# Kernel optimization log

Hardware: AMD Instinct MI355X
Metric: run time of the kernel (lower is better)

Reference implementation:

```python
import jax, jax.numpy as jnp
import numpy as np

N_NODES = 1_000_000
HID = 64
BATCH = 262_144


def _gru_cell(x, h, w_ih, w_hh, b_ih, b_hh):
    # PyTorch GRUCell semantics. w_ih/w_hh: [3H, H]; gate order r, z, n.
    gi = x @ w_ih.T + b_ih
    gh = h @ w_hh.T + b_hh
    i_r, i_z, i_n = jnp.split(gi, 3, axis=-1)
    h_r, h_z, h_n = jnp.split(gh, 3, axis=-1)
    r = jax.nn.sigmoid(i_r + h_r)
    z = jax.nn.sigmoid(i_z + h_z)
    n = jnp.tanh(i_n + r * h_n)
    return (1.0 - z) * n + z * h


def setup_inputs() -> dict:
    key = jax.random.key(0)
    ks = jax.random.split(key, 16)
    H = HID
    s = lambda fan_in: 1.0 / np.sqrt(fan_in)
    return {
        "node_pairs": jax.random.randint(ks[0], (BATCH, 2), 0, N_NODES, dtype=jnp.int64)
        if jax.config.jax_enable_x64 else jax.random.randint(ks[0], (BATCH, 2), 0, N_NODES, dtype=jnp.int32),
        "memory": jax.random.normal(ks[1], (N_NODES, H), dtype=jnp.float32),
        "msg_w1": jax.random.uniform(ks[2], (H, 2 * H), jnp.float32, -s(2 * H), s(2 * H)),
        "msg_b1": jax.random.uniform(ks[3], (H,), jnp.float32, -s(2 * H), s(2 * H)),
        "msg_w2": jax.random.uniform(ks[4], (H, H), jnp.float32, -s(H), s(H)),
        "msg_b2": jax.random.uniform(ks[5], (H,), jnp.float32, -s(H), s(H)),
        "gru_w_ih": jax.random.uniform(ks[6], (3 * H, H), jnp.float32, -s(H), s(H)),
        "gru_w_hh": jax.random.uniform(ks[7], (3 * H, H), jnp.float32, -s(H), s(H)),
        "gru_b_ih": jax.random.uniform(ks[8], (3 * H,), jnp.float32, -s(H), s(H)),
        "gru_b_hh": jax.random.uniform(ks[9], (3 * H,), jnp.float32, -s(H), s(H)),
        "lp_w1": jax.random.uniform(ks[10], (H, 2 * H), jnp.float32, -s(2 * H), s(2 * H)),
        "lp_b1": jax.random.uniform(ks[11], (H,), jnp.float32, -s(2 * H), s(2 * H)),
        "lp_w2": jax.random.uniform(ks[12], (1, H), jnp.float32, -s(H), s(H)),
        "lp_b2": jax.random.uniform(ks[13], (1,), jnp.float32, -s(H), s(H)),
    }


def reference(node_pairs, memory, msg_w1, msg_b1, msg_w2, msg_b2,
              gru_w_ih, gru_w_hh, gru_b_ih, gru_b_hh,
              lp_w1, lp_b1, lp_w2, lp_b2):
    n1_mem = memory[node_pairs[:, 0]]  # [B, H]
    n2_mem = memory[node_pairs[:, 1]]  # [B, H]
    x = jnp.concatenate([n1_mem, n2_mem], axis=1)  # [B, 2H]
    messages = jax.nn.relu(x @ msg_w1.T + msg_b1) @ msg_w2.T + msg_b2  # [B, H]
    n1_upd = _gru_cell(messages, n1_mem, gru_w_ih, gru_w_hh, gru_b_ih, gru_b_hh)
    n2_upd = _gru_cell(messages, n2_mem, gru_w_ih, gru_w_hh, gru_b_ih, gru_b_hh)
    combined = jnp.concatenate([n1_upd, n2_upd], axis=1)  # [B, 2H]
    h = jax.nn.relu(combined @ lp_w1.T + lp_b1)  # dropout inactive in eval
    out = jax.nn.sigmoid(h @ lp_w2.T + lp_b2)  # [B, 1]
    return out.squeeze(-1)
```

## Files before the change

kernel.cpp:

```cpp
#include <hip/hip_runtime.h>

#define BATCH 262144

typedef __attribute__((ext_vector_type(8))) short short8;
typedef __attribute__((ext_vector_type(4))) float f32x4;

static __device__ __forceinline__ unsigned cvtpk(float lo, float hi) {
    unsigned r;
    asm("v_cvt_pk_bf16_f32 %0, %1, %2" : "=v"(r) : "v"(lo), "v"(hi));
    return r;
}
static __device__ __forceinline__ unsigned short f2b(float f) {
    unsigned u = __float_as_uint(f);
    return (unsigned short)((u + 0x7fffu + ((u >> 16) & 1u)) >> 16);
}
static __device__ __forceinline__ float b2f(short s) {
    return __uint_as_float(((unsigned)(unsigned short)s) << 16);
}
static __device__ __forceinline__ float sigm(float x) { return 1.0f / (1.0f + __expf(-x)); }
static __device__ __forceinline__ float tanh_f(float x) { return 1.0f - 2.0f / (__expf(2.0f * x) + 1.0f); }

#define WAVE_FENCE() asm volatile("" ::: "memory")

static __device__ __forceinline__ int sw128(int row, int cb) { return row * 128 + (cb ^ ((row & 7) << 4)); }
static __device__ __forceinline__ int sw256(int row, int cb) { return row * 256 + (cb ^ ((row & 7) << 4)); }

__global__ void prep_weights(const float* __restrict__ w1, const float* __restrict__ w2,
                             const float* __restrict__ wih, const float* __restrict__ whh,
                             const float* __restrict__ lw1, unsigned short* __restrict__ wsb) {
    int i = blockIdx.x * 256 + threadIdx.x;
    float v;
    if (i < 8192) v = w1[i];
    else if (i < 12288) v = w2[i - 8192];
    else if (i < 24576) v = wih[i - 12288];
    else if (i < 36864) v = whh[i - 24576];
    else if (i < 45056) v = lw1[i - 36864];
    else return;
    wsb[i] = f2b(v);
}

#define WLDS_BYTES 90112
#define NCHUNK (WLDS_BYTES / 16)

__global__ __launch_bounds__(768) void tgn_kernel(
    const int* __restrict__ pairs, const float* __restrict__ memory,
    const unsigned short* __restrict__ wsb,
    const float* __restrict__ b1, const float* __restrict__ b2,
    const float* __restrict__ bih, const float* __restrict__ bhh,
    const float* __restrict__ lb1, const float* __restrict__ lw2,
    const float* __restrict__ lb2, float* __restrict__ out)
{
    __shared__ __align__(16) char wlds[WLDS_BYTES];
    __shared__ __align__(16) char work[12][6144];

    const int tid = threadIdx.x;
    const int w  = tid >> 6;
    const int l  = tid & 63;
    const int lr = l & 15;
    const int lg = l >> 4;

    for (int c = tid; c < NCHUNK; c += 768) {
        int byte = c * 16;
        int base, sh;
        if (byte < 16384)      { base = 0;     sh = 8; }
        else if (byte < 24576) { base = 16384; sh = 7; }
        else if (byte < 49152) { base = 24576; sh = 7; }
        else if (byte < 73728) { base = 49152; sh = 7; }
        else                   { base = 73728; sh = 8; }
        int t   = byte - base;
        int row = t >> sh;
        int dst = base + (t ^ ((row & 7) << 4));
        *(short8*)(wlds + dst) = *(const short8*)((const char*)wsb + byte);
    }
    __syncthreads();

    char* n1b = &work[w][0];
    char* n2b = &work[w][2048];
    char* hmb = &work[w][4096];

    const char* w1l  = wlds + 0;
    const char* w2l  = wlds + 16384;
    const char* wihl = wlds + 24576;
    const char* whhl = wlds + 49152;
    const char* lw1l = wlds + 73728;

    const f32x4 z4 = {0.0f, 0.0f, 0.0f, 0.0f};

    const int waveid = blockIdx.x * 12 + w;

    int2 pr[4];
#pragma unroll
    for (int rr = 0; rr < 4; ++rr)
        pr[rr] = *(const int2*)(pairs + (waveid * 16 + rr * 4 + lg) * 2);

#pragma unroll 1
    for (int tile = waveid; tile < 16384; tile += 3072) {
        const int r0 = tile * 16;

#pragma unroll
        for (int rr = 0; rr < 4; ++rr) {
            int row = rr * 4 + lg;
            f32x4 v1 = *(const f32x4*)(memory + (long)pr[rr].x * 64 + lr * 4);
            f32x4 v2 = *(const f32x4*)(memory + (long)pr[rr].y * 64 + lr * 4);
            uint2 c1v, c2v;
            c1v.x = cvtpk(v1[0], v1[1]); c1v.y = cvtpk(v1[2], v1[3]);
            c2v.x = cvtpk(v2[0], v2[1]); c2v.y = cvtpk(v2[2], v2[3]);
            int off = sw128(row, lr * 8);
            *(uint2*)(n1b + off) = c1v;
            *(uint2*)(n2b + off) = c2v;
        }
        {
            int next = tile + 3072;
            if (next < 16384) {
#pragma unroll
                for (int rr = 0; rr < 4; ++rr)
                    pr[rr] = *(const int2*)(pairs + (next * 16 + rr * 4 + lg) * 2);
            }
        }
        WAVE_FENCE();

        f32x4 acc[4];
#pragma unroll
        for (int nt = 0; nt < 4; ++nt) acc[nt] = z4;
#pragma unroll
        for (int kt = 0; kt < 4; ++kt) {
            const char* base = (kt < 2) ? n1b : n2b;
            short8 a = *(const short8*)(base + sw128(lr, (kt & 1) * 64 + lg * 16));
#pragma unroll
            for (int nt = 0; nt < 4; ++nt) {
                short8 b = *(const short8*)(w1l + sw256(nt * 16 + lr, kt * 64 + lg * 16));
                acc[nt] = __builtin_amdgcn_mfma_f32_16x16x32_bf16(a, b, acc[nt], 0, 0, 0);
            }
        }
#pragma unroll
        for (int nt = 0; nt < 4; ++nt) {
            float bv = b1[nt * 16 + lr];
            unsigned p01 = cvtpk(fmaxf(acc[nt][0] + bv, 0.0f), fmaxf(acc[nt][1] + bv, 0.0f));
            unsigned p23 = cvtpk(fmaxf(acc[nt][2] + bv, 0.0f), fmaxf(acc[nt][3] + bv, 0.0f));
            int cb = nt * 32 + lr * 2;
            *(short*)(hmb + sw128(lg * 4 + 0, cb)) = (short)p01;
            *(short*)(hmb + sw128(lg * 4 + 1, cb)) = (short)(p01 >> 16);
            *(short*)(hmb + sw128(lg * 4 + 2, cb)) = (short)p23;
            *(short*)(hmb + sw128(lg * 4 + 3, cb)) = (short)(p23 >> 16);
        }
        WAVE_FENCE();

#pragma unroll
        for (int nt = 0; nt < 4; ++nt) acc[nt] = z4;
#pragma unroll
        for (int kt = 0; kt < 2; ++kt) {
            short8 a = *(const short8*)(hmb + sw128(lr, kt * 64 + lg * 16));
#pragma unroll
            for (int nt = 0; nt < 4; ++nt) {
                short8 b = *(const short8*)(w2l + sw128(nt * 16 + lr, kt * 64 + lg * 16));
                acc[nt] = __builtin_amdgcn_mfma_f32_16x16x32_bf16(a, b, acc[nt], 0, 0, 0);
            }
        }
#pragma unroll
        for (int nt = 0; nt < 4; ++nt) {
            float bv = b2[nt * 16 + lr];
            unsigned p01 = cvtpk(acc[nt][0] + bv, acc[nt][1] + bv);
            unsigned p23 = cvtpk(acc[nt][2] + bv, acc[nt][3] + bv);
            int cb = nt * 32 + lr * 2;
            *(short*)(hmb + sw128(lg * 4 + 0, cb)) = (short)p01;
            *(short*)(hmb + sw128(lg * 4 + 1, cb)) = (short)(p01 >> 16);
            *(short*)(hmb + sw128(lg * 4 + 2, cb)) = (short)p23;
            *(short*)(hmb + sw128(lg * 4 + 3, cb)) = (short)(p23 >> 16);
        }
        WAVE_FENCE();

        short8 am[2], a1[2], a2[2];
#pragma unroll
        for (int kt = 0; kt < 2; ++kt) {
            am[kt] = *(const short8*)(hmb + sw128(lr, kt * 64 + lg * 16));
            a1[kt] = *(const short8*)(n1b + sw128(lr, kt * 64 + lg * 16));
            a2[kt] = *(const short8*)(n2b + sw128(lr, kt * 64 + lg * 16));
        }
#pragma unroll
        for (int nt = 0; nt < 4; ++nt) {
            f32x4 gir = z4, giz = z4, gin = z4;
            f32x4 g1r = z4, g1z = z4, g1n = z4;
            f32x4 g2r = z4, g2z = z4, g2n = z4;
#pragma unroll
            for (int kt = 0; kt < 2; ++kt) {
                int ko = kt * 64 + lg * 16;
                short8 bir = *(const short8*)(wihl + sw128((0 + nt) * 16 + lr, ko));
                short8 biz = *(const short8*)(wihl + sw128((4 + nt) * 16 + lr, ko));
                short8 bin = *(const short8*)(wihl + sw128((8 + nt) * 16 + lr, ko));
                short8 bhr = *(const short8*)(whhl + sw128((0 + nt) * 16 + lr, ko));
                short8 bhz = *(const short8*)(whhl + sw128((4 + nt) * 16 + lr, ko));
                short8 bhn = *(const short8*)(whhl + sw128((8 + nt) * 16 + lr, ko));
                gir = __builtin_amdgcn_mfma_f32_16x16x32_bf16(am[kt], bir, gir, 0, 0, 0);
                giz = __builtin_amdgcn_mfma_f32_16x16x32_bf16(am[kt], biz, giz, 0, 0, 0);
                gin = __builtin_amdgcn_mfma_f32_16x16x32_bf16(am[kt], bin, gin, 0, 0, 0);
                g1r = __builtin_amdgcn_mfma_f32_16x16x32_bf16(a1[kt], bhr, g1r, 0, 0, 0);
                g1z = __builtin_amdgcn_mfma_f32_16x16x32_bf16(a1[kt], bhz, g1z, 0, 0, 0);
                g1n = __builtin_amdgcn_mfma_f32_16x16x32_bf16(a1[kt], bhn, g1n, 0, 0, 0);
                g2r = __builtin_amdgcn_mfma_f32_16x16x32_bf16(a2[kt], bhr, g2r, 0, 0, 0);
                g2z = __builtin_amdgcn_mfma_f32_16x16x32_bf16(a2[kt], bhz, g2z, 0, 0, 0);
                g2n = __builtin_amdgcn_mfma_f32_16x16x32_bf16(a2[kt], bhn, g2n, 0, 0, 0);
            }
            int j = nt * 16 + lr;
            float bir_ = bih[j], biz_ = bih[64 + j], bin_ = bih[128 + j];
            float bhr_ = bhh[j], bhz_ = bhh[64 + j], bhn_ = bhh[128 + j];
            float o1[4], o2[4];
#pragma unroll
            for (int r = 0; r < 4; ++r) {
                int row = lg * 4 + r;
                float i_r = gir[r] + bir_;
                float i_z = giz[r] + biz_;
                float i_n = gin[r] + bin_;
                float rg = sigm(i_r + g1r[r] + bhr_);
                float zg = sigm(i_z + g1z[r] + bhz_);
                float ng = tanh_f(i_n + rg * (g1n[r] + bhn_));
                float h  = b2f(*(const short*)(n1b + sw128(row, j * 2)));
                o1[r] = (1.0f - zg) * ng + zg * h;
                rg = sigm(i_r + g2r[r] + bhr_);
                zg = sigm(i_z + g2z[r] + bhz_);
                ng = tanh_f(i_n + rg * (g2n[r] + bhn_));
                h  = b2f(*(const short*)(n2b + sw128(row, j * 2)));
                o2[r] = (1.0f - zg) * ng + zg * h;
            }
            unsigned q01 = cvtpk(o1[0], o1[1]), q23 = cvtpk(o1[2], o1[3]);
            unsigned s01 = cvtpk(o2[0], o2[1]), s23 = cvtpk(o2[2], o2[3]);
            *(short*)(n1b + sw128(lg * 4 + 0, j * 2)) = (short)q01;
            *(short*)(n1b + sw128(lg * 4 + 1, j * 2)) = (short)(q01 >> 16);
            *(short*)(n1b + sw128(lg * 4 + 2, j * 2)) = (short)q23;
            *(short*)(n1b + sw128(lg * 4 + 3, j * 2)) = (short)(q23 >> 16);
            *(short*)(n2b + sw128(lg * 4 + 0, j * 2)) = (short)s01;
            *(short*)(n2b + sw128(lg * 4 + 1, j * 2)) = (short)(s01 >> 16);
            *(short*)(n2b + sw128(lg * 4 + 2, j * 2)) = (short)s23;
            *(short*)(n2b + sw128(lg * 4 + 3, j * 2)) = (short)(s23 >> 16);
        }
        WAVE_FENCE();

        f32x4 acc5[4];
#pragma unroll
        for (int nt = 0; nt < 4; ++nt) acc5[nt] = z4;
#pragma unroll
        for (int kt = 0; kt < 4; ++kt) {
            const char* base = (kt < 2) ? n1b : n2b;
            short8 a = *(const short8*)(base + sw128(lr, (kt & 1) * 64 + lg * 16));
#pragma unroll
            for (int nt = 0; nt < 4; ++nt) {
                short8 b = *(const short8*)(lw1l + sw256(nt * 16 + lr, kt * 64 + lg * 16));
                acc5[nt] = __builtin_amdgcn_mfma_f32_16x16x32_bf16(a, b, acc5[nt], 0, 0, 0);
            }
        }

        float part[4] = {0.0f, 0.0f, 0.0f, 0.0f};
#pragma unroll
        for (int nt = 0; nt < 4; ++nt) {
            float w2v = lw2[nt * 16 + lr];
            float bv  = lb1[nt * 16 + lr];
#pragma unroll
            for (int r = 0; r < 4; ++r)
                part[r] += fmaxf(acc5[nt][r] + bv, 0.0f) * w2v;
        }
        float lb2v = lb2[0];
#pragma unroll
        for (int r = 0; r < 4; ++r) {
            float p = part[r];
            p += __shfl_xor(p, 1);
            p += __shfl_xor(p, 2);
            p += __shfl_xor(p, 4);
            p += __shfl_xor(p, 8);
            if (lr == 0) out[r0 + lg * 4 + r] = sigm(p + lb2v);
        }
    }
}

extern "C" void kernel_launch(void* const* d_in, const int* in_sizes, int n_in,
                              void* d_out, int out_size, void* d_ws, size_t ws_size,
                              hipStream_t stream) {
    const int*   pairs  = (const int*)d_in[0];
    const float* memory = (const float*)d_in[1];
    const float* w1  = (const float*)d_in[2];
    const float* b1  = (const float*)d_in[3];
    const float* w2  = (const float*)d_in[4];
    const float* b2  = (const float*)d_in[5];
    const float* wih = (const float*)d_in[6];
    const float* whh = (const float*)d_in[7];
    const float* bih = (const float*)d_in[8];
    const float* bhh = (const float*)d_in[9];
    const float* lw1 = (const float*)d_in[10];
    const float* lb1 = (const float*)d_in[11];
    const float* lw2 = (const float*)d_in[12];
    const float* lb2 = (const float*)d_in[13];
    unsigned short* wsb = (unsigned short*)d_ws;

    prep_weights<<<176, 256, 0, stream>>>(w1, w2, wih, whh, lw1, wsb);
    tgn_kernel<<<256, 768, 0, stream>>>(pairs, memory, wsb, b1, b2, bih, bhh,
                                        lb1, lw2, lb2, (float*)d_out);
}
```

Before: 110.6 us.

## Shrink per-wave LDS scratch to two buffers and run 16 waves per block

Each wave's LDS scratch drops from three 2 KB buffers to two by keeping the bf16 node-memory A fragments in registers and reusing the buffers for the MLP and GRU intermediates. The GRU blend term h is now re-read from global fp32 memory instead of the bf16 LDS copy. That frees enough LDS to launch 1024-thread blocks, so more waves run concurrently to hide gather latency. The costs are extra scattered global loads of memory rows, plus pair indices, in the GRU epilogue, and higher register pressure.

```diff
diff --git a/kernel.cpp b/kernel.cpp
--- a/kernel.cpp
+++ b/kernel.cpp
@@ -13,9 +13,6 @@
 static __device__ __forceinline__ unsigned short f2b(float f) {
     unsigned u = __float_as_uint(f);
     return (unsigned short)((u + 0x7fffu + ((u >> 16) & 1u)) >> 16);
-}
-static __device__ __forceinline__ float b2f(short s) {
-    return __uint_as_float(((unsigned)(unsigned short)s) << 16);
 }
 static __device__ __forceinline__ float sigm(float x) { return 1.0f / (1.0f + __expf(-x)); }
 static __device__ __forceinline__ float tanh_f(float x) { return 1.0f - 2.0f / (__expf(2.0f * x) + 1.0f); }
@@ -42,7 +39,7 @@
 #define WLDS_BYTES 90112
 #define NCHUNK (WLDS_BYTES / 16)
 
-__global__ __launch_bounds__(768) void tgn_kernel(
+__global__ __launch_bounds__(1024) void tgn_kernel(
     const int* __restrict__ pairs, const float* __restrict__ memory,
     const unsigned short* __restrict__ wsb,
     const float* __restrict__ b1, const float* __restrict__ b2,
@@ -51,7 +48,7 @@
     const float* __restrict__ lb2, float* __restrict__ out)
 {
     __shared__ __align__(16) char wlds[WLDS_BYTES];
-    __shared__ __align__(16) char work[12][6144];
+    __shared__ __align__(16) char work[16][4096];
 
     const int tid = threadIdx.x;
     const int w  = tid >> 6;
@@ -59,7 +56,7 @@
     const int lr = l & 15;
     const int lg = l >> 4;
 
-    for (int c = tid; c < NCHUNK; c += 768) {
+    for (int c = tid; c < NCHUNK; c += 1024) {
         int byte = c * 16;
         int base, sh;
         if (byte < 16384)      { base = 0;     sh = 8; }
@@ -74,9 +71,8 @@
     }
     __syncthreads();
 
-    char* n1b = &work[w][0];
-    char* n2b = &work[w][2048];
-    char* hmb = &work[w][4096];
+    char* buf0 = &work[w][0];
+    char* buf1 = &work[w][2048];
 
     const char* w1l  = wlds + 0;
     const char* w2l  = wlds + 16384;
@@ -86,7 +82,7 @@
 
     const f32x4 z4 = {0.0f, 0.0f, 0.0f, 0.0f};
 
-    const int waveid = blockIdx.x * 12 + w;
+    const int waveid = blockIdx.x * 16 + w;
 
     int2 pr[4];
 #pragma unroll
@@ -94,7 +90,7 @@
         pr[rr] = *(const int2*)(pairs + (waveid * 16 + rr * 4 + lg) * 2);
 
 #pragma unroll 1
-    for (int tile = waveid; tile < 16384; tile += 3072) {
+    for (int tile = waveid; tile < 16384; tile += 4096) {
         const int r0 = tile * 16;
 
 #pragma unroll
@@ -106,11 +102,15 @@
             c1v.x = cvtpk(v1[0], v1[1]); c1v.y = cvtpk(v1[2], v1[3]);
             c2v.x = cvtpk(v2[0], v2[1]); c2v.y = cvtpk(v2[2], v2[3]);
             int off = sw128(row, lr * 8);
-            *(uint2*)(n1b + off) = c1v;
-            *(uint2*)(n2b + off) = c2v;
-        }
+            *(uint2*)(buf0 + off) = c1v;
+            *(uint2*)(buf1 + off) = c2v;
+        }
+        int2 hpr[4];
+#pragma unroll
+        for (int r = 0; r < 4; ++r)
+            hpr[r] = *(const int2*)(pairs + (r0 + lg * 4 + r) * 2);
         {
-            int next = tile + 3072;
+            int next = tile + 4096;
             if (next < 16384) {
 #pragma unroll
                 for (int rr = 0; rr < 4; ++rr)
@@ -119,13 +119,19 @@
         }
         WAVE_FENCE();
 
+        short8 x1[2], x2[2];
+#pragma unroll
+        for (int kt = 0; kt < 2; ++kt) {
+            x1[kt] = *(const short8*)(buf0 + sw128(lr, kt * 64 + lg * 16));
+            x2[kt] = *(const short8*)(buf1 + sw128(lr, kt * 64 + lg * 16));
+        }
+        WAVE_FENCE();
         f32x4 acc[4];
 #pragma unroll
         for (int nt = 0; nt < 4; ++nt) acc[nt] = z4;
 #pragma unroll
         for (int kt = 0; kt < 4; ++kt) {
-            const char* base = (kt < 2) ? n1b : n2b;
-            short8 a = *(const short8*)(base + sw128(lr, (kt & 1) * 64 + lg * 16));
+            short8 a = (kt == 0) ? x1[0] : (kt == 1) ? x1[1] : (kt == 2) ? x2[0] : x2[1];
 #pragma unroll
             for (int nt = 0; nt < 4; ++nt) {
                 short8 b = *(const short8*)(w1l + sw256(nt * 16 + lr, kt * 64 + lg * 16));
@@ -138,10 +144,10 @@
             unsigned p01 = cvtpk(fmaxf(acc[nt][0] + bv, 0.0f), fmaxf(acc[nt][1] + bv, 0.0f));
             unsigned p23 = cvtpk(fmaxf(acc[nt][2] + bv, 0.0f), fmaxf(acc[nt][3] + bv, 0.0f));
             int cb = nt * 32 + lr * 2;
-            *(short*)(hmb + sw128(lg * 4 + 0, cb)) = (short)p01;
-            *(short*)(hmb + sw128(lg * 4 + 1, cb)) = (short)(p01 >> 16);
-            *(short*)(hmb + sw128(lg * 4 + 2, cb)) = (short)p23;
-            *(short*)(hmb + sw128(lg * 4 + 3, cb)) = (short)(p23 >> 16);
+            *(short*)(buf0 + sw128(lg * 4 + 0, cb)) = (short)p01;
+            *(short*)(buf0 + sw128(lg * 4 + 1, cb)) = (short)(p01 >> 16);
+            *(short*)(buf0 + sw128(lg * 4 + 2, cb)) = (short)p23;
+            *(short*)(buf0 + sw128(lg * 4 + 3, cb)) = (short)(p23 >> 16);
         }
         WAVE_FENCE();
 
@@ -149,7 +155,7 @@
         for (int nt = 0; nt < 4; ++nt) acc[nt] = z4;
 #pragma unroll
         for (int kt = 0; kt < 2; ++kt) {
-            short8 a = *(const short8*)(hmb + sw128(lr, kt * 64 + lg * 16));
+            short8 a = *(const short8*)(buf0 + sw128(lr, kt * 64 + lg * 16));
 #pragma unroll
             for (int nt = 0; nt < 4; ++nt) {
                 short8 b = *(const short8*)(w2l + sw128(nt * 16 + lr, kt * 64 + lg * 16));
@@ -162,20 +168,17 @@
             unsigned p01 = cvtpk(acc[nt][0] + bv, acc[nt][1] + bv);
             unsigned p23 = cvtpk(acc[nt][2] + bv, acc[nt][3] + bv);
             int cb = nt * 32 + lr * 2;
-            *(short*)(hmb + sw128(lg * 4 + 0, cb)) = (short)p01;
-            *(short*)(hmb + sw128(lg * 4 + 1, cb)) = (short)(p01 >> 16);
-            *(short*)(hmb + sw128(lg * 4 + 2, cb)) = (short)p23;
-            *(short*)(hmb + sw128(lg * 4 + 3, cb)) = (short)(p23 >> 16);
-        }
-        WAVE_FENCE();
-
-        short8 am[2], a1[2], a2[2];
-#pragma unroll
-        for (int kt = 0; kt < 2; ++kt) {
-            am[kt] = *(const short8*)(hmb + sw128(lr, kt * 64 + lg * 16));
-            a1[kt] = *(const short8*)(n1b + sw128(lr, kt * 64 + lg * 16));
-            a2[kt] = *(const short8*)(n2b + sw128(lr, kt * 64 + lg * 16));
-        }
+            *(short*)(buf1 + sw128(lg * 4 + 0, cb)) = (short)p01;
+            *(short*)(buf1 + sw128(lg * 4 + 1, cb)) = (short)(p01 >> 16);
+            *(short*)(buf1 + sw128(lg * 4 + 2, cb)) = (short)p23;
+            *(short*)(buf1 + sw128(lg * 4 + 3, cb)) = (short)(p23 >> 16);
+        }
+        WAVE_FENCE();
+
+        short8 am[2];
+        am[0] = *(const short8*)(buf1 + sw128(lr, lg * 16));
+        am[1] = *(const short8*)(buf1 + sw128(lr, 64 + lg * 16));
+        WAVE_FENCE();
 #pragma unroll
         for (int nt = 0; nt < 4; ++nt) {
             f32x4 gir = z4, giz = z4, gin = z4;
@@ -190,15 +193,16 @@
                 short8 bhr = *(const short8*)(whhl + sw128((0 + nt) * 16 + lr, ko));
                 short8 bhz = *(const short8*)(whhl + sw128((4 + nt) * 16 + lr, ko));
                 short8 bhn = *(const short8*)(whhl + sw128((8 + nt) * 16 + lr, ko));
+                short8 a1k = x1[kt], a2k = x2[kt];
                 gir = __builtin_amdgcn_mfma_f32_16x16x32_bf16(am[kt], bir, gir, 0, 0, 0);
                 giz = __builtin_amdgcn_mfma_f32_16x16x32_bf16(am[kt], biz, giz, 0, 0, 0);
                 gin = __builtin_amdgcn_mfma_f32_16x16x32_bf16(am[kt], bin, gin, 0, 0, 0);
-                g1r = __builtin_amdgcn_mfma_f32_16x16x32_bf16(a1[kt], bhr, g1r, 0, 0, 0);
-                g1z = __builtin_amdgcn_mfma_f32_16x16x32_bf16(a1[kt], bhz, g1z, 0, 0, 0);
-                g1n = __builtin_amdgcn_mfma_f32_16x16x32_bf16(a1[kt], bhn, g1n, 0, 0, 0);
-                g2r = __builtin_amdgcn_mfma_f32_16x16x32_bf16(a2[kt], bhr, g2r, 0, 0, 0);
-                g2z = __builtin_amdgcn_mfma_f32_16x16x32_bf16(a2[kt], bhz, g2z, 0, 0, 0);
-                g2n = __builtin_amdgcn_mfma_f32_16x16x32_bf16(a2[kt], bhn, g2n, 0, 0, 0);
+                g1r = __builtin_amdgcn_mfma_f32_16x16x32_bf16(a1k, bhr, g1r, 0, 0, 0);
+                g1z = __builtin_amdgcn_mfma_f32_16x16x32_bf16(a1k, bhz, g1z, 0, 0, 0);
+                g1n = __builtin_amdgcn_mfma_f32_16x16x32_bf16(a1k, bhn, g1n, 0, 0, 0);
+                g2r = __builtin_amdgcn_mfma_f32_16x16x32_bf16(a2k, bhr, g2r, 0, 0, 0);
+                g2z = __builtin_amdgcn_mfma_f32_16x16x32_bf16(a2k, bhz, g2z, 0, 0, 0);
+                g2n = __builtin_amdgcn_mfma_f32_16x16x32_bf16(a2k, bhn, g2n, 0, 0, 0);
             }
             int j = nt * 16 + lr;
             float bir_ = bih[j], biz_ = bih[64 + j], bin_ = bih[128 + j];
@@ -206,31 +210,30 @@
             float o1[4], o2[4];
 #pragma unroll
             for (int r = 0; r < 4; ++r) {
-                int row = lg * 4 + r;
                 float i_r = gir[r] + bir_;
                 float i_z = giz[r] + biz_;
                 float i_n = gin[r] + bin_;
+                float h1v = memory[(long)hpr[r].x * 64 + j];
+                float h2v = memory[(long)hpr[r].y * 64 + j];
                 float rg = sigm(i_r + g1r[r] + bhr_);
                 float zg = sigm(i_z + g1z[r] + bhz_);
                 float ng = tanh_f(i_n + rg * (g1n[r] + bhn_));
-                float h  = b2f(*(const short*)(n1b + sw128(row, j * 2)));
-                o1[r] = (1.0f - zg) * ng + zg * h;
+                o1[r] = (1.0f - zg) * ng + zg * h1v;
                 rg = sigm(i_r + g2r[r] + bhr_);
                 zg = sigm(i_z + g2z[r] + bhz_);
                 ng = tanh_f(i_n + rg * (g2n[r] + bhn_));
-                h  = b2f(*(const short*)(n2b + sw128(row, j * 2)));
-                o2[r] = (1.0f - zg) * ng + zg * h;
+                o2[r] = (1.0f - zg) * ng + zg * h2v;
             }
             unsigned q01 = cvtpk(o1[0], o1[1]), q23 = cvtpk(o1[2], o1[3]);
             unsigned s01 = cvtpk(o2[0], o2[1]), s23 = cvtpk(o2[2], o2[3]);
-            *(short*)(n1b + sw128(lg * 4 + 0, j * 2)) = (short)q01;
-            *(short*)(n1b + sw128(lg * 4 + 1, j * 2)) = (short)(q01 >> 16);
-            *(short*)(n1b + sw128(lg * 4 + 2, j * 2)) = (short)q23;
-            *(short*)(n1b + sw128(lg * 4 + 3, j * 2)) = (short)(q23 >> 16);
-            *(short*)(n2b + sw128(lg * 4 + 0, j * 2)) = (short)s01;
-            *(short*)(n2b + sw128(lg * 4 + 1, j * 2)) = (short)(s01 >> 16);
-            *(short*)(n2b + sw128(lg * 4 + 2, j * 2)) = (short)s23;
-            *(short*)(n2b + sw128(lg * 4 + 3, j * 2)) = (short)(s23 >> 16);
+            *(short*)(buf0 + sw128(lg * 4 + 0, j * 2)) = (short)q01;
+            *(short*)(buf0 + sw128(lg * 4 + 1, j * 2)) = (short)(q01 >> 16);
+            *(short*)(buf0 + sw128(lg * 4 + 2, j * 2)) = (short)q23;
+            *(short*)(buf0 + sw128(lg * 4 + 3, j * 2)) = (short)(q23 >> 16);
+            *(short*)(buf1 + sw128(lg * 4 + 0, j * 2)) = (short)s01;
+            *(short*)(buf1 + sw128(lg * 4 + 1, j * 2)) = (short)(s01 >> 16);
+            *(short*)(buf1 + sw128(lg * 4 + 2, j * 2)) = (short)s23;
+            *(short*)(buf1 + sw128(lg * 4 + 3, j * 2)) = (short)(s23 >> 16);
         }
         WAVE_FENCE();
 
@@ -239,7 +242,7 @@
         for (int nt = 0; nt < 4; ++nt) acc5[nt] = z4;
 #pragma unroll
         for (int kt = 0; kt < 4; ++kt) {
-            const char* base = (kt < 2) ? n1b : n2b;
+            const char* base = (kt < 2) ? buf0 : buf1;
             short8 a = *(const short8*)(base + sw128(lr, (kt & 1) * 64 + lg * 16));
 #pragma unroll
             for (int nt = 0; nt < 4; ++nt) {
@@ -290,6 +293,6 @@
     unsigned short* wsb = (unsigned short*)d_ws;
 
     prep_weights<<<176, 256, 0, stream>>>(w1, w2, wih, whh, lw1, wsb);
-    tgn_kernel<<<256, 768, 0, stream>>>(pairs, memory, wsb, b1, b2, bih, bhh,
-                                        lb1, lw2, lb2, (float*)d_out);
-}
+    tgn_kernel<<<256, 1024, 0, stream>>>(pairs, memory, wsb, b1, b2, bih, bhh,
+                                         lb1, lw2, lb2, (float*)d_out);
+}
```

After: 155.0 us. 40.2% more time.
